# Kernel tuning notes

Measured on AMD Instinct MI355X. Metric: run time of the kernel, lower is better.

Reference implementation:

```python
import jax, jax.numpy as jnp
import numpy as np

N_HEADS = 16
ROPE_BASE = 10000.0


def _apply_rope(t, cos, sin):
    # t: (B, H, S, D); cos/sin: (S, D/2). Rotate-half convention.
    d2 = t.shape[-1] // 2
    t1, t2 = t[..., :d2], t[..., d2:]
    return jnp.concatenate([t1 * cos - t2 * sin, t2 * cos + t1 * sin], axis=-1)


def setup_inputs() -> dict:
    key = jax.random.key(0)
    k0, k1, k2, k3, k4 = jax.random.split(key, 5)
    B, S, E = 4, 2048, 1024
    scale = 0.02
    x = jax.random.normal(k0, (B, S, E), dtype=jnp.float32)
    w_qkv = jax.random.normal(k1, (E, 3 * E), dtype=jnp.float32) * scale
    b_qkv = jnp.zeros((3 * E,), dtype=jnp.float32)
    w_proj = jax.random.normal(k2, (E, E), dtype=jnp.float32) * scale
    b_proj = jnp.zeros((E,), dtype=jnp.float32)
    return {"x": x, "w_qkv": w_qkv, "b_qkv": b_qkv, "w_proj": w_proj, "b_proj": b_proj}


def reference(x, w_qkv, b_qkv, w_proj, b_proj):
    B, S, E = x.shape
    H = N_HEADS
    D = E // H
    # fused QKV projection
    qkv = x @ w_qkv + b_qkv                      # (B, S, 3E)
    q, k, v = jnp.split(qkv, 3, axis=-1)
    def to_heads(t):
        return t.reshape(B, S, H, D).transpose(0, 2, 1, 3)  # (B, H, S, D)
    q, k, v = to_heads(q), to_heads(k), to_heads(v)
    # RoPE (rotate-half)
    inv_freq = ROPE_BASE ** (-jnp.arange(0, D, 2, dtype=jnp.float32) / D)  # (D/2,)
    pos = jnp.arange(S, dtype=jnp.float32)
    freqs = pos[:, None] * inv_freq[None, :]     # (S, D/2)
    cos, sin = jnp.cos(freqs), jnp.sin(freqs)
    q = _apply_rope(q, cos, sin)
    k = _apply_rope(k, cos, sin)
    # causal SDPA
    scores = jnp.einsum('bhqd,bhkd->bhqk', q, k) / jnp.sqrt(jnp.float32(D))
    causal = jnp.tril(jnp.ones((S, S), dtype=bool))
    scores = jnp.where(causal, scores, jnp.float32(-1e30))
    probs = jax.nn.softmax(scores, axis=-1)
    out = jnp.einsum('bhqk,bhkd->bhqd', probs, v)  # (B, H, S, D)
    out = out.transpose(0, 2, 1, 3).reshape(B, S, E)
    # output projection (dropout is identity at p=0 / eval)
    return out @ w_proj + b_proj
```

## Files before the change

kernel.cpp:

```cpp
#include <hip/hip_runtime.h>

typedef unsigned short u16;
typedef __bf16 bf16x8 __attribute__((ext_vector_type(8)));
typedef float f32x4 __attribute__((ext_vector_type(4)));

__device__ __forceinline__ u16 f2b(float f) {
    unsigned u = __builtin_bit_cast(unsigned, f);
    unsigned r = (u + 0x7fffu + ((u >> 16) & 1u)) >> 16;
    return (u16)r;
}
#if __has_builtin(__builtin_amdgcn_cvt_pk_bf16_f32)
typedef __bf16 bf16x2_t __attribute__((ext_vector_type(2)));
__device__ __forceinline__ unsigned pk2(float a, float b) {
    return __builtin_bit_cast(unsigned, __builtin_amdgcn_cvt_pk_bf16_f32(a, b));
}
#else
__device__ __forceinline__ unsigned pk2(float a, float b) {
    return (unsigned)f2b(a) | ((unsigned)f2b(b) << 16);
}
#endif
#if __has_builtin(__builtin_amdgcn_exp2f)
#define EXP2F(x) __builtin_amdgcn_exp2f(x)
#else
#define EXP2F(x) exp2f(x)
#endif

__device__ __forceinline__ void gl_lds16(const u16* g, u16* l) {
    __builtin_amdgcn_global_load_lds(
        (const __attribute__((address_space(1))) unsigned*)(const void*)g,
        (__attribute__((address_space(3))) unsigned*)(void*)l, 16, 0, 0);
}

__global__ __launch_bounds__(256) void k_rope_table(float2* __restrict__ tab) {
    int i = blockIdx.x * 256 + threadIdx.x;
    int s = i >> 5, d = i & 31;
    const float C0 = 0.4152410118609203f;
    float inv_freq = exp2f(-C0 * (float)d);
    float sn, cs;
    sincosf((float)s * inv_freq, &sn, &cs);
    tab[i] = make_float2(cs, sn);
}

__global__ __launch_bounds__(256) void k_convert(const float* __restrict__ in,
                                                 u16* __restrict__ out, int n8) {
    int i = blockIdx.x * 256 + threadIdx.x;
    if (i >= n8) return;
    const float4* p = (const float4*)(in + (size_t)i * 8);
    float4 a = p[0], b = p[1];
    u16 t[8] = {f2b(a.x), f2b(a.y), f2b(a.z), f2b(a.w),
                f2b(b.x), f2b(b.y), f2b(b.z), f2b(b.w)};
    *(uint4*)(out + (size_t)i * 8) = *(const uint4*)t;
}

__global__ __launch_bounds__(256) void k_transpose_bf16(const float* __restrict__ in,
                                                        u16* __restrict__ out,
                                                        int R, int C) {
    __shared__ u16 tile[64][72];
    int tc = blockIdx.x * 64;
    int tr = blockIdx.y * 64;
    for (int i = threadIdx.x; i < 4096; i += 256) {
        int r = i >> 6, c = i & 63;
        tile[c][r] = f2b(in[(size_t)(tr + r) * C + tc + c]);
    }
    __syncthreads();
    for (int i = threadIdx.x; i < 4096; i += 256) {
        int r = i >> 6, c = i & 63;
        out[(size_t)(tc + r) * R + tr + c] = tile[r][c];
    }
}

__device__ __forceinline__ void gemm_mainloop(const u16* __restrict__ Ab,
                                              const u16* __restrict__ Bb, int K,
                                              u16* As, u16* Bs, int tid,
                                              f32x4 (&acc)[4][4]) {
    const int wave = tid >> 6, lane = tid & 63;
    const int col = lane & 15, quad = lane >> 4;
    const int wm = wave >> 1, wn = wave & 1;
    const int lrow = lane >> 2, lk = (lane & 3) * 8;
    u16* ldsA0 = As + (wave * 16) * 32;
    u16* ldsA1 = As + (64 + wave * 16) * 32;
    u16* ldsB0 = Bs + (wave * 16) * 32;
    u16* ldsB1 = Bs + (64 + wave * 16) * 32;
    const u16* gA0 = Ab + (size_t)(wave * 16 + lrow) * K + lk;
    const u16* gA1 = gA0 + (size_t)64 * K;
    const u16* gB0 = Bb + (size_t)(wave * 16 + lrow) * K + lk;
    const u16* gB1 = gB0 + (size_t)64 * K;
    for (int k0 = 0; k0 < K; k0 += 64) {
        if (k0) __syncthreads();
#pragma unroll
        for (int kh = 0; kh < 2; ++kh) {
            int ko = k0 + kh * 32;
            gl_lds16(gA0 + ko, ldsA0 + kh * 4096);
            gl_lds16(gA1 + ko, ldsA1 + kh * 4096);
            gl_lds16(gB0 + ko, ldsB0 + kh * 4096);
            gl_lds16(gB1 + ko, ldsB1 + kh * 4096);
        }
        __syncthreads();
#pragma unroll
        for (int kh = 0; kh < 2; ++kh) {
            bf16x8 af[4], bfr[4];
#pragma unroll
            for (int mt = 0; mt < 4; ++mt)
                af[mt] = *(const bf16x8*)(As + kh * 4096 +
                                          (wm * 64 + mt * 16 + col) * 32 + quad * 8);
#pragma unroll
            for (int nt = 0; nt < 4; ++nt)
                bfr[nt] = *(const bf16x8*)(Bs + kh * 4096 +
                                           (wn * 64 + nt * 16 + col) * 32 + quad * 8);
#pragma unroll
            for (int mt = 0; mt < 4; ++mt)
#pragma unroll
                for (int nt = 0; nt < 4; ++nt)
                    acc[mt][nt] = __builtin_amdgcn_mfma_f32_16x16x32_bf16(
                        af[mt], bfr[nt], acc[mt][nt], 0, 0, 0);
        }
    }
}

__global__ __launch_bounds__(256) void k_gemm_qkv_rope(
    const u16* __restrict__ A, const u16* __restrict__ Bt,
    const float* __restrict__ bias, const float2* __restrict__ tab,
    u16* __restrict__ Qr, u16* __restrict__ Kr, u16* __restrict__ Vt) {
    __shared__ __align__(16) u16 smem[16384];
    u16* As = smem;
    u16* Bs = smem + 8192;
    const int K = 1024;
    int tid = threadIdx.x;
    int lane = tid & 63, wave = tid >> 6;
    int col = lane & 15, quad = lane >> 4;
    int wm = wave >> 1, wn = wave & 1;
    int mBase = blockIdx.y * 128;
    int nBase = blockIdx.x * 128;
    f32x4 acc[4][4] = {};
    gemm_mainloop(A + (size_t)mBase * K, Bt + (size_t)nBase * K, K, As, Bs, tid, acc);

    int region = nBase >> 10;
    int n64 = nBase + wn * 64;
    int h = (n64 & 1023) >> 6;
    if (region < 2) {
        __syncthreads();
        float qs = (region == 0) ? 0.18033688011112042f : 1.0f;
#pragma unroll
        for (int nt = 0; nt < 2; ++nt) {
            int d1 = nt * 16 + col;
            float b1 = bias[n64 + d1];
            float b2 = bias[n64 + d1 + 32];
            int nl = wn * 64 + nt * 16 + col;
#pragma unroll
            for (int mt = 0; mt < 4; ++mt) {
                int mlb = wm * 64 + mt * 16 + quad * 4;
#pragma unroll
                for (int r = 0; r < 4; ++r) {
                    int mloc = mlb + r;
                    int s = (mBase + mloc) & 2047;
                    float2 t = tab[s * 32 + d1];
                    float t1 = acc[mt][nt][r] + b1;
                    float t2 = acc[mt][nt + 2][r] + b2;
                    int sw = (mloc & 7) << 3;
                    smem[mloc * 128 + (nl ^ sw)] = f2b((t1 * t.x - t2 * t.y) * qs);
                    smem[mloc * 128 + ((nl + 32) ^ sw)] = f2b((t2 * t.x + t1 * t.y) * qs);
                }
            }
        }
        __syncthreads();
        u16* outp = (region == 0) ? Qr : Kr;
#pragma unroll
        for (int p = 0; p < 8; ++p) {
            int lin = p * 256 + tid;
            int mloc = lin >> 4;
            int c8 = (lin & 15) << 3;
            uint4 v = *(const uint4*)(smem + mloc * 128 + (c8 ^ ((mloc & 7) << 3)));
            int m = mBase + mloc;
            int s = m & 2047, b = m >> 11;
            int ng = (nBase & 1023) + c8;
            *(uint4*)(Qr == outp || Kr == outp
                          ? outp + ((size_t)((b * 16 + (ng >> 6)) * 2048 + s)) * 64 +
                                (ng & 63)
                          : outp) = v;
        }
    } else {
        int b = mBase >> 11;
        int sb0 = mBase & 2047;
#pragma unroll
        for (int nt = 0; nt < 4; ++nt) {
            int d = nt * 16 + col;
            float bv = bias[n64 + d];
            u16* vrow = Vt + ((size_t)((b * 16 + h) * 64 + d)) * 2048;
#pragma unroll
            for (int mt = 0; mt < 4; ++mt) {
                int s = sb0 + wm * 64 + mt * 16 + quad * 4;
                uint2 w;
                w.x = pk2(acc[mt][nt][0] + bv, acc[mt][nt][1] + bv);
                w.y = pk2(acc[mt][nt][2] + bv, acc[mt][nt][3] + bv);
                *(uint2*)(vrow + s) = w;
            }
        }
    }
}

__global__ __launch_bounds__(256, 4) void k_attn(const u16* __restrict__ Qr,
                                                 const u16* __restrict__ Kr,
                                                 const u16* __restrict__ Vt,
                                                 u16* __restrict__ O) {
    __shared__ __align__(16) u16 Ks[2][64 * 72];
    __shared__ __align__(16) u16 Vs[2][64 * 72];
    int tid = threadIdx.x, wave = tid >> 6, lane = tid & 63;
    int col = lane & 15, quad = lane >> 4;
    int id = blockIdx.x + (blockIdx.y << 4);
    int xcd = id & 7, w = id >> 3;
    int head = xcd * 8 + (w & 7);
    int tsel = w >> 3;
    int b = head >> 4, h = head & 15;
    size_t headQ = (size_t)head * 2048 * 64;
    size_t headV = (size_t)head * 64 * 2048;
    int r0 = tid >> 3, kc = tid & 7;
    int rb72 = ((col >> 2) * 8 + (col & 3)) * 72;
    const u16* kg0 = Kr + headQ + (size_t)r0 * 64 + kc * 8;
    const u16* vg0 = Vt + headV + (size_t)r0 * 2048 + kc * 8;

#pragma unroll 1
    for (int phase = 0; phase < 2; ++phase) {
        int T = phase ? tsel : 31 - tsel;
        int myq = T * 64 + wave * 16 + col;
        const u16* qp = Qr + headQ + (size_t)myq * 64;
        bf16x8 aq0 = *(const bf16x8*)(qp + quad * 8);
        bf16x8 aq1 = *(const bf16x8*)(qp + 32 + quad * 8);
        f32x4 o[4] = {};
        float l = 0.f;

        __syncthreads();
        {
            uint4 a0 = *(const uint4*)kg0;
            uint4 a1 = *(const uint4*)(kg0 + 32 * 64);
            uint4 v0 = *(const uint4*)vg0;
            uint4 v1 = *(const uint4*)(vg0 + 32 * 2048);
            *(uint4*)(Ks[0] + r0 * 72 + kc * 8) = a0;
            *(uint4*)(Ks[0] + (r0 + 32) * 72 + kc * 8) = a1;
            *(uint4*)(Vs[0] + r0 * 72 + kc * 8) = v0;
            *(uint4*)(Vs[0] + (r0 + 32) * 72 + kc * 8) = v1;
        }
        __syncthreads();

        for (int j = 0; j <= T; ++j) {
            int cur = j & 1;
            uint4 kr0, kr1, vr0, vr1;
            if (j < T) {
                const u16* kgn = kg0 + (size_t)(j + 1) * 64 * 64;
                const u16* vgn = vg0 + (j + 1) * 64;
                kr0 = *(const uint4*)kgn;
                kr1 = *(const uint4*)(kgn + 32 * 64);
                vr0 = *(const uint4*)vgn;
                vr1 = *(const uint4*)(vgn + 32 * 2048);
            }
            const u16* KsC = Ks[cur];
            const u16* VsC = Vs[cur];
            f32x4 s[4];
#pragma unroll
            for (int nt = 0; nt < 4; ++nt) {
                const u16* kp = KsC + rb72 + ((nt & 1) * 32 + (nt >> 1) * 4) * 72;
                bf16x8 ak0 = *(const bf16x8*)(kp + quad * 8);
                bf16x8 ak1 = *(const bf16x8*)(kp + 32 + quad * 8);
                f32x4 z = {};
                z = __builtin_amdgcn_mfma_f32_16x16x32_bf16(ak0, aq0, z, 0, 0, 0);
                s[nt] = __builtin_amdgcn_mfma_f32_16x16x32_bf16(ak1, aq1, z, 0, 0, 0);
            }
            if (j == T) {
#pragma unroll
                for (int nt = 0; nt < 4; ++nt) {
                    int keyb = j * 64 + (nt & 1) * 32 + quad * 8 + (nt >> 1) * 4;
#pragma unroll
                    for (int r = 0; r < 4; ++r)
                        if (keyb + r > myq) s[nt][r] = -3.0e38f;
                }
            }
            unsigned P4[8];
#pragma unroll
            for (int nt = 0; nt < 4; ++nt) {
                float p0 = EXP2F(s[nt][0]);
                float p1 = EXP2F(s[nt][1]);
                float p2 = EXP2F(s[nt][2]);
                float p3 = EXP2F(s[nt][3]);
                l += (p0 + p1) + (p2 + p3);
                P4[2 * nt] = pk2(p0, p1);
                P4[2 * nt + 1] = pk2(p2, p3);
            }
#pragma unroll
            for (int kk = 0; kk < 2; ++kk) {
                uint4 bw;
                bw.x = P4[2 * kk];
                bw.y = P4[2 * kk + 1];
                bw.z = P4[2 * kk + 4];
                bw.w = P4[2 * kk + 5];
                bf16x8 bp = __builtin_bit_cast(bf16x8, bw);
#pragma unroll
                for (int mt = 0; mt < 4; ++mt) {
                    bf16x8 av = *(const bf16x8*)(VsC + (mt * 16 + col) * 72 + kk * 32 + quad * 8);
                    o[mt] = __builtin_amdgcn_mfma_f32_16x16x32_bf16(av, bp, o[mt], 0, 0, 0);
                }
            }
            if (j < T) {
                int nxt = cur ^ 1;
                *(uint4*)(Ks[nxt] + r0 * 72 + kc * 8) = kr0;
                *(uint4*)(Ks[nxt] + (r0 + 32) * 72 + kc * 8) = kr1;
                *(uint4*)(Vs[nxt] + r0 * 72 + kc * 8) = vr0;
                *(uint4*)(Vs[nxt] + (r0 + 32) * 72 + kc * 8) = vr1;
                __syncthreads();
            }
        }
        l += __shfl_xor(l, 16);
        l += __shfl_xor(l, 32);
        float inv = 1.0f / l;
        u16* orow = O + (size_t)(b * 2048 + myq) * 1024 + h * 64;
#pragma unroll
        for (int mt = 0; mt < 4; ++mt) {
            uint2 w2;
            w2.x = pk2(o[mt][0] * inv, o[mt][1] * inv);
            w2.y = pk2(o[mt][2] * inv, o[mt][3] * inv);
            *(uint2*)(orow + mt * 16 + quad * 4) = w2;
        }
    }
}

__global__ __launch_bounds__(256) void k_gemm_proj(const u16* __restrict__ A,
                                                   const u16* __restrict__ Bt,
                                                   const float* __restrict__ bias,
                                                   float* __restrict__ out) {
    __shared__ __align__(16) u16 As[2 * 128 * 32];
    __shared__ __align__(16) u16 Bs[2 * 128 * 32];
    const int K = 1024;
    int tid = threadIdx.x;
    int lane = tid & 63, wave = tid >> 6;
    int col = lane & 15, quad = lane >> 4;
    int wm = wave >> 1, wn = wave & 1;
    int mBase = blockIdx.y * 128;
    int nBase = blockIdx.x * 128;
    f32x4 acc[4][4] = {};
    gemm_mainloop(A + (size_t)mBase * K, Bt + (size_t)nBase * K, K, As, Bs, tid, acc);
#pragma unroll
    for (int nt = 0; nt < 4; ++nt) {
        int n = nBase + wn * 64 + nt * 16 + col;
        float bv = bias[n];
#pragma unroll
        for (int mt = 0; mt < 4; ++mt) {
            int m = mBase + wm * 64 + mt * 16 + quad * 4;
#pragma unroll
            for (int r = 0; r < 4; ++r)
                out[(size_t)(m + r) * 1024 + n] = acc[mt][nt][r] + bv;
        }
    }
}

extern "C" void kernel_launch(void* const* d_in, const int* in_sizes, int n_in,
                              void* d_out, int out_size, void* d_ws, size_t ws_size,
                              hipStream_t stream) {
    const float* x = (const float*)d_in[0];
    const float* w_qkv = (const float*)d_in[1];
    const float* b_qkv = (const float*)d_in[2];
    const float* w_proj = (const float*)d_in[3];
    const float* b_proj = (const float*)d_in[4];
    float* out = (float*)d_out;
    char* ws = (char*)d_ws;
    u16* x_bf = (u16*)(ws);
    u16* wqkvT = (u16*)(ws + 16777216);
    u16* wprojT = (u16*)(ws + 23068672);
    u16* Qr = (u16*)(ws + 25165824);
    u16* Kr = (u16*)(ws + 41943040);
    u16* Vt = (u16*)(ws + 58720256);
    u16* AO = (u16*)(ws + 75497472);
    float2* tab = (float2*)(ws + 75497472);

    k_rope_table<<<256, 256, 0, stream>>>(tab);
    k_convert<<<4096, 256, 0, stream>>>(x, x_bf, 1048576);
    k_transpose_bf16<<<dim3(48, 16), 256, 0, stream>>>(w_qkv, wqkvT, 1024, 3072);
    k_transpose_bf16<<<dim3(16, 16), 256, 0, stream>>>(w_proj, wprojT, 1024, 1024);
    k_gemm_qkv_rope<<<dim3(24, 64), 256, 0, stream>>>(x_bf, wqkvT, b_qkv, tab, Qr, Kr, Vt);
    k_attn<<<dim3(16, 64), 256, 0, stream>>>(Qr, Kr, Vt, AO);
    k_gemm_proj<<<dim3(8, 64), 256, 0, stream>>>(AO, wprojT, b_proj, out);
}
```

Baseline: 256.3 us.

## Fuse prep kernels and stage attention K/V via direct global-to-LDS swizzled loads

Merges the rope-table, input-convert and two weight-transpose kernels into one launch, removing three launch gaps. In attention, K/V tiles are now copied with global_load_lds straight into XOR-swizzled unpadded LDS instead of a register round trip into padded rows. The MFMA sections are wrapped in s_setprio. This frees registers and overlaps the next tile's load with compute, but depends on the async LDS writes completing before the unconditional per-iteration barrier and on the swizzle matching the reads.

```diff
diff --git a/kernel.cpp b/kernel.cpp
--- a/kernel.cpp
+++ b/kernel.cpp
@@ -31,41 +31,50 @@
         (__attribute__((address_space(3))) unsigned*)(void*)l, 16, 0, 0);
 }
 
-__global__ __launch_bounds__(256) void k_rope_table(float2* __restrict__ tab) {
-    int i = blockIdx.x * 256 + threadIdx.x;
-    int s = i >> 5, d = i & 31;
-    const float C0 = 0.4152410118609203f;
-    float inv_freq = exp2f(-C0 * (float)d);
-    float sn, cs;
-    sincosf((float)s * inv_freq, &sn, &cs);
-    tab[i] = make_float2(cs, sn);
-}
-
-__global__ __launch_bounds__(256) void k_convert(const float* __restrict__ in,
-                                                 u16* __restrict__ out, int n8) {
-    int i = blockIdx.x * 256 + threadIdx.x;
-    if (i >= n8) return;
-    const float4* p = (const float4*)(in + (size_t)i * 8);
-    float4 a = p[0], b = p[1];
-    u16 t[8] = {f2b(a.x), f2b(a.y), f2b(a.z), f2b(a.w),
-                f2b(b.x), f2b(b.y), f2b(b.z), f2b(b.w)};
-    *(uint4*)(out + (size_t)i * 8) = *(const uint4*)t;
-}
-
-__global__ __launch_bounds__(256) void k_transpose_bf16(const float* __restrict__ in,
-                                                        u16* __restrict__ out,
-                                                        int R, int C) {
-    __shared__ u16 tile[64][72];
-    int tc = blockIdx.x * 64;
-    int tr = blockIdx.y * 64;
-    for (int i = threadIdx.x; i < 4096; i += 256) {
+__device__ __forceinline__ void transpose64(const float* __restrict__ in,
+                                            u16* __restrict__ out, int R, int C,
+                                            int tr, int tc, int tid, u16 (*tile)[72]) {
+    for (int i = tid; i < 4096; i += 256) {
         int r = i >> 6, c = i & 63;
         tile[c][r] = f2b(in[(size_t)(tr + r) * C + tc + c]);
     }
     __syncthreads();
-    for (int i = threadIdx.x; i < 4096; i += 256) {
+    for (int i = tid; i < 4096; i += 256) {
         int r = i >> 6, c = i & 63;
         out[(size_t)(tc + r) * R + tr + c] = tile[r][c];
+    }
+}
+
+__global__ __launch_bounds__(256) void k_prep(const float* __restrict__ x,
+                                              u16* __restrict__ x_bf,
+                                              const float* __restrict__ w_qkv,
+                                              u16* __restrict__ wqkvT,
+                                              const float* __restrict__ w_proj,
+                                              u16* __restrict__ wprojT,
+                                              float2* __restrict__ tab) {
+    __shared__ u16 tile[64][72];
+    int bid = blockIdx.x, tid = threadIdx.x;
+    if (bid < 4096) {
+        int i = bid * 256 + tid;
+        const float4* p = (const float4*)(x + (size_t)i * 8);
+        float4 a = p[0], b = p[1];
+        u16 t[8] = {f2b(a.x), f2b(a.y), f2b(a.z), f2b(a.w),
+                    f2b(b.x), f2b(b.y), f2b(b.z), f2b(b.w)};
+        *(uint4*)(x_bf + (size_t)i * 8) = *(const uint4*)t;
+    } else if (bid < 4864) {
+        int q = bid - 4096;
+        transpose64(w_qkv, wqkvT, 1024, 3072, (q / 48) * 64, (q % 48) * 64, tid, tile);
+    } else if (bid < 5120) {
+        int q = bid - 4864;
+        transpose64(w_proj, wprojT, 1024, 1024, (q / 16) * 64, (q % 16) * 64, tid, tile);
+    } else {
+        int i = (bid - 5120) * 256 + tid;
+        int s = i >> 5, d = i & 31;
+        const float C0 = 0.4152410118609203f;
+        float inv_freq = exp2f(-C0 * (float)d);
+        float sn, cs;
+        sincosf((float)s * inv_freq, &sn, &cs);
+        tab[i] = make_float2(cs, sn);
     }
 }
 
@@ -198,12 +207,33 @@
     }
 }
 
+__device__ __forceinline__ void stage_kv(const u16* __restrict__ Kt,
+                                         const u16* __restrict__ Vtb,
+                                         u16* KsB, u16* VsB, int wave, int lane) {
+    int lr = lane >> 3;
+    int lc = lane & 7;
+#pragma unroll
+    for (int i = 0; i < 2; ++i) {
+        int s = wave * 2 + i;
+        int r = s * 8 + lr;
+        int key = (r & 3) | (((r >> 3) & 1) << 2);
+        gl_lds16(Kt + (size_t)r * 64 + ((lc ^ key) << 3), KsB + s * 512);
+    }
+#pragma unroll
+    for (int i = 0; i < 2; ++i) {
+        int s = wave * 2 + i;
+        int d = s * 8 + lr;
+        int key = d & 7;
+        gl_lds16(Vtb + (size_t)d * 2048 + ((lc ^ key) << 3), VsB + s * 512);
+    }
+}
+
 __global__ __launch_bounds__(256, 4) void k_attn(const u16* __restrict__ Qr,
                                                  const u16* __restrict__ Kr,
                                                  const u16* __restrict__ Vt,
                                                  u16* __restrict__ O) {
-    __shared__ __align__(16) u16 Ks[2][64 * 72];
-    __shared__ __align__(16) u16 Vs[2][64 * 72];
+    __shared__ __align__(16) u16 Ks[2][4096];
+    __shared__ __align__(16) u16 Vs[2][4096];
     int tid = threadIdx.x, wave = tid >> 6, lane = tid & 63;
     int col = lane & 15, quad = lane >> 4;
     int id = blockIdx.x + (blockIdx.y << 4);
@@ -213,10 +243,8 @@
     int b = head >> 4, h = head & 15;
     size_t headQ = (size_t)head * 2048 * 64;
     size_t headV = (size_t)head * 64 * 2048;
-    int r0 = tid >> 3, kc = tid & 7;
-    int rb72 = ((col >> 2) * 8 + (col & 3)) * 72;
-    const u16* kg0 = Kr + headQ + (size_t)r0 * 64 + kc * 8;
-    const u16* vg0 = Vt + headV + (size_t)r0 * 2048 + kc * 8;
+    int prow = (col >> 2) * 8 + (col & 3);
+    int ck = col & 7;
 
 #pragma unroll 1
     for (int phase = 0; phase < 2; ++phase) {
@@ -228,42 +256,29 @@
         f32x4 o[4] = {};
         float l = 0.f;
 
-        __syncthreads();
-        {
-            uint4 a0 = *(const uint4*)kg0;
-            uint4 a1 = *(const uint4*)(kg0 + 32 * 64);
-            uint4 v0 = *(const uint4*)vg0;
-            uint4 v1 = *(const uint4*)(vg0 + 32 * 2048);
-            *(uint4*)(Ks[0] + r0 * 72 + kc * 8) = a0;
-            *(uint4*)(Ks[0] + (r0 + 32) * 72 + kc * 8) = a1;
-            *(uint4*)(Vs[0] + r0 * 72 + kc * 8) = v0;
-            *(uint4*)(Vs[0] + (r0 + 32) * 72 + kc * 8) = v1;
-        }
+        stage_kv(Kr + headQ, Vt + headV, Ks[0], Vs[0], wave, lane);
         __syncthreads();
 
         for (int j = 0; j <= T; ++j) {
             int cur = j & 1;
-            uint4 kr0, kr1, vr0, vr1;
-            if (j < T) {
-                const u16* kgn = kg0 + (size_t)(j + 1) * 64 * 64;
-                const u16* vgn = vg0 + (j + 1) * 64;
-                kr0 = *(const uint4*)kgn;
-                kr1 = *(const uint4*)(kgn + 32 * 64);
-                vr0 = *(const uint4*)vgn;
-                vr1 = *(const uint4*)(vgn + 32 * 2048);
-            }
+            if (j < T)
+                stage_kv(Kr + headQ + ((size_t)(j + 1) << 12),
+                         Vt + headV + (j + 1) * 64, Ks[cur ^ 1], Vs[cur ^ 1],
+                         wave, lane);
             const u16* KsC = Ks[cur];
             const u16* VsC = Vs[cur];
             f32x4 s[4];
+            __builtin_amdgcn_s_setprio(1);
 #pragma unroll
             for (int nt = 0; nt < 4; ++nt) {
-                const u16* kp = KsC + rb72 + ((nt & 1) * 32 + (nt >> 1) * 4) * 72;
-                bf16x8 ak0 = *(const bf16x8*)(kp + quad * 8);
-                bf16x8 ak1 = *(const bf16x8*)(kp + 32 + quad * 8);
+                const u16* kp = KsC + ((nt & 1) * 32 + (nt >> 1) * 4 + prow) * 64;
+                bf16x8 ak0 = *(const bf16x8*)(kp + ((quad ^ ck) << 3));
+                bf16x8 ak1 = *(const bf16x8*)(kp + (((quad + 4) ^ ck) << 3));
                 f32x4 z = {};
                 z = __builtin_amdgcn_mfma_f32_16x16x32_bf16(ak0, aq0, z, 0, 0, 0);
                 s[nt] = __builtin_amdgcn_mfma_f32_16x16x32_bf16(ak1, aq1, z, 0, 0, 0);
             }
+            __builtin_amdgcn_s_setprio(0);
             if (j == T) {
 #pragma unroll
                 for (int nt = 0; nt < 4; ++nt) {
@@ -284,6 +299,7 @@
                 P4[2 * nt] = pk2(p0, p1);
                 P4[2 * nt + 1] = pk2(p2, p3);
             }
+            __builtin_amdgcn_s_setprio(1);
 #pragma unroll
             for (int kk = 0; kk < 2; ++kk) {
                 uint4 bw;
@@ -294,18 +310,13 @@
                 bf16x8 bp = __builtin_bit_cast(bf16x8, bw);
 #pragma unroll
                 for (int mt = 0; mt < 4; ++mt) {
-                    bf16x8 av = *(const bf16x8*)(VsC + (mt * 16 + col) * 72 + kk * 32 + quad * 8);
+                    bf16x8 av = *(const bf16x8*)(VsC + (mt * 16 + col) * 64 +
+                                                 (((kk * 4 + quad) ^ ck) << 3));
                     o[mt] = __builtin_amdgcn_mfma_f32_16x16x32_bf16(av, bp, o[mt], 0, 0, 0);
                 }
             }
-            if (j < T) {
-                int nxt = cur ^ 1;
-                *(uint4*)(Ks[nxt] + r0 * 72 + kc * 8) = kr0;
-                *(uint4*)(Ks[nxt] + (r0 + 32) * 72 + kc * 8) = kr1;
-                *(uint4*)(Vs[nxt] + r0 * 72 + kc * 8) = vr0;
-                *(uint4*)(Vs[nxt] + (r0 + 32) * 72 + kc * 8) = vr1;
-                __syncthreads();
-            }
+            __builtin_amdgcn_s_setprio(0);
+            __syncthreads();
         }
         l += __shfl_xor(l, 16);
         l += __shfl_xor(l, 32);
@@ -369,10 +380,7 @@
     u16* AO = (u16*)(ws + 75497472);
     float2* tab = (float2*)(ws + 75497472);
 
-    k_rope_table<<<256, 256, 0, stream>>>(tab);
-    k_convert<<<4096, 256, 0, stream>>>(x, x_bf, 1048576);
-    k_transpose_bf16<<<dim3(48, 16), 256, 0, stream>>>(w_qkv, wqkvT, 1024, 3072);
-    k_transpose_bf16<<<dim3(16, 16), 256, 0, stream>>>(w_proj, wprojT, 1024, 1024);
+    k_prep<<<5376, 256, 0, stream>>>(x, x_bf, w_qkv, wqkvT, w_proj, wprojT, tab);
     k_gemm_qkv_rope<<<dim3(24, 64), 256, 0, stream>>>(x_bf, wqkvT, b_qkv, tab, Qr, Kr, Vt);
     k_attn<<<dim3(16, 64), 256, 0, stream>>>(Qr, Kr, Vt, AO);
     k_gemm_proj<<<dim3(8, 64), 256, 0, stream>>>(AO, wprojT, b_proj, out);
```

Result: faster. 244.7 us (-4.5%).
